# Kernel optimization log

Measured on AMD Instinct MI355X. Metric: run time of the kernel, lower is better.

## Reference

```python
import jax, jax.numpy as jnp
import numpy as np

N = 50000      # nodes
E = 800000     # edges (before self loops)
F_IN = 128     # input feature dim
H = 4          # attention heads
C = 64         # per-head channels (hidden_dim = out_channels = 64)
HC = H * C     # 256, concat output width of each GATv2Conv
G = 32         # number of graphs in the batch
NEG_SLOPE_ATT = 0.2   # GATv2 internal LeakyReLU
NEG_SLOPE_ACT = 0.01  # encoder nn.LeakyReLU() default


def _glorot(key, shape, fan_in):
    return jax.random.normal(key, shape, jnp.float32) * (1.0 / np.sqrt(fan_in))


def setup_inputs() -> dict:
    key = jax.random.key(0)
    ks = jax.random.split(key, 32)
    inp = {}
    inp["x"] = jax.random.normal(ks[0], (N, F_IN), jnp.float32)
    inp["edge_index"] = jax.random.randint(ks[1], (2, E), 0, N, jnp.int32)
    inp["batch"] = jnp.sort(jax.random.randint(ks[2], (N,), 0, G, jnp.int32))
    i = 3
    for li, fin in ((1, F_IN), (2, HC), (3, HC)):
        inp[f"Wl{li}"] = _glorot(ks[i], (HC, fin), fin); i += 1
        inp[f"bl{li}"] = jnp.zeros((HC,), jnp.float32)
        inp[f"Wr{li}"] = _glorot(ks[i], (HC, fin), fin); i += 1
        inp[f"br{li}"] = jnp.zeros((HC,), jnp.float32)
        inp[f"att{li}"] = _glorot(ks[i], (H, C), C); i += 1
        inp[f"bo{li}"] = jnp.zeros((HC,), jnp.float32)
    return inp


def _gatv2_layer(x, src, dst, Wl, bl, Wr, br, att, bo):
    n = x.shape[0]
    xl = (x @ Wl.T + bl).reshape(n, H, C)  # source transform
    xr = (x @ Wr.T + br).reshape(n, H, C)  # target transform
    # per-edge attention logits: a^T LeakyReLU(xl[j] + xr[i])
    e = jax.nn.leaky_relu(xl[src] + xr[dst], negative_slope=NEG_SLOPE_ATT)  # [E', H, C]
    score = jnp.einsum('ehc,hc->eh', e, att)                                # [E', H]
    # segment softmax over incoming edges of each destination node
    m = jax.ops.segment_max(score, dst, num_segments=n)
    p = jnp.exp(score - m[dst])
    s = jax.ops.segment_sum(p, dst, num_segments=n)
    alpha = p / s[dst]
    out = jax.ops.segment_sum(alpha[:, :, None] * xl[src], dst, num_segments=n)
    return out.reshape(n, HC) + bo


def reference(x, edge_index, batch,
              Wl1, bl1, Wr1, br1, att1, bo1,
              Wl2, bl2, Wr2, br2, att2, bo2,
              Wl3, bl3, Wr3, br3, att3, bo3):
    loop = jnp.arange(N, dtype=edge_index.dtype)
    src = jnp.concatenate([edge_index[0], loop])  # add self loops (PyG default)
    dst = jnp.concatenate([edge_index[1], loop])
    h = _gatv2_layer(x, src, dst, Wl1, bl1, Wr1, br1, att1, bo1)
    h = jax.nn.leaky_relu(h, negative_slope=NEG_SLOPE_ACT)
    h = _gatv2_layer(h, src, dst, Wl2, bl2, Wr2, br2, att2, bo2)
    h = jax.nn.leaky_relu(h, negative_slope=NEG_SLOPE_ACT)
    h = _gatv2_layer(h, src, dst, Wl3, bl3, Wr3, br3, att3, bo3)
    # global mean pool over graphs
    sums = jax.ops.segment_sum(h, batch, num_segments=G)
    cnt = jax.ops.segment_sum(jnp.ones((N,), h.dtype), batch, num_segments=G)
    return sums / jnp.maximum(cnt, 1.0)[:, None]
```

## Files before the change

kernel.cpp:

```cpp
#include <hip/hip_runtime.h>

#define HEADS 4
#define CH 64
#define HC 256
#define NGRAPH 32
#define NEG_ATT 0.2f
#define NEG_ACT 0.01f

typedef __attribute__((ext_vector_type(8))) short bf16x8;
typedef __attribute__((ext_vector_type(4))) float f32x4;

typedef __attribute__((address_space(3))) unsigned int lds_u32;
typedef const __attribute__((address_space(1))) unsigned int glob_u32;

__device__ __forceinline__ void gl_lds16(const void* g, void* l) {
  __builtin_amdgcn_global_load_lds((glob_u32*)(uintptr_t)g,
                                   (lds_u32*)(unsigned int)(uintptr_t)l, 16, 0, 0);
}

__device__ __forceinline__ void split2(float a, float b, unsigned& hi, unsigned& lo) {
  unsigned ua = __float_as_uint(a), ub = __float_as_uint(b);
  float la = a - __uint_as_float(ua & 0xFFFF0000u);
  float lb = b - __uint_as_float(ub & 0xFFFF0000u);
  hi = __builtin_amdgcn_perm(ub, ua, 0x07060302u);
  lo = __builtin_amdgcn_perm(__float_as_uint(lb), __float_as_uint(la), 0x07060302u);
}

__device__ __forceinline__ unsigned rtn_bf16(float f) {
  unsigned u = __float_as_uint(f);
  return (u + 0x7FFFu + ((u >> 16) & 1u)) >> 16;
}

__global__ __launch_bounds__(256) void convert_x(
    const float* __restrict__ X, unsigned short* __restrict__ xhi,
    unsigned short* __restrict__ xlo, int total4) {
  int g = blockIdx.x * 256 + threadIdx.x;
  if (g >= total4) return;
  float4 v = *(const float4*)&X[(size_t)g * 4];
  uint2 h2, l2;
  split2(v.x, v.y, h2.x, l2.x);
  split2(v.z, v.w, h2.y, l2.y);
  *(uint2*)&xhi[(size_t)g * 4] = h2;
  *(uint2*)&xlo[(size_t)g * 4] = l2;
}

__global__ __launch_bounds__(256) void convert_w_frag(
    const float* __restrict__ Wl, const float* __restrict__ Wr,
    unsigned short* __restrict__ wfhi, unsigned short* __restrict__ wflo, int K) {
  int g = blockIdx.x * 256 + threadIdx.x;
  int lane = g & 63;
  int ct = (g >> 6) & 31;
  int kb = g >> 11;
  int col = ct * 16 + (lane & 15);
  int k = kb * 32 + (lane >> 4) * 8;
  const float* src = (col < HC) ? &Wl[(size_t)col * K + k] : &Wr[(size_t)(col - HC) * K + k];
  float4 v0 = *(const float4*)src;
  float4 v1 = *(const float4*)(src + 4);
  uint4 hq, lq;
  split2(v0.x, v0.y, hq.x, lq.x);
  split2(v0.z, v0.w, hq.y, lq.y);
  split2(v1.x, v1.y, hq.z, lq.z);
  split2(v1.z, v1.w, hq.w, lq.w);
  *(uint4*)&wfhi[(size_t)g * 8] = hq;
  *(uint4*)&wflo[(size_t)g * 8] = lq;
}

__global__ __launch_bounds__(256) void gemm_fused(
    const unsigned short* __restrict__ xhi, const unsigned short* __restrict__ xlo,
    const unsigned short* __restrict__ wfhi, const unsigned short* __restrict__ wflo,
    const float* __restrict__ bl, const float* __restrict__ br,
    unsigned short* __restrict__ Y1, float* __restrict__ Y2, int N, int K) {
  __shared__ unsigned short Ah[2][128][32];
  __shared__ unsigned short Al[2][128][32];

  const int tid = threadIdx.x;
  const int wave = tid >> 6;
  const int lane = tid & 63;
  const int quad = lane >> 4;
  const int l16 = lane & 15;
  const int wr = (wave >> 1) * 64;
  const int wc = (wave & 1) * 64;
  const int col0 = blockIdx.x * 128;
  const int row0 = blockIdx.y * 128;
  const int ctg0 = blockIdx.x * 8 + (wave & 1) * 4;
  const int nkb = K >> 5;

  const int c0 = tid, c1 = tid + 256;
  const int r0g = row0 + (c0 >> 2), r1g = row0 + (c1 >> 2);
  const int ko0 = (c0 & 3) * 8, ko1 = (c1 & 3) * 8;
  const int gr0 = (r0g < N) ? r0g : N - 1;
  const int gr1 = (r1g < N) ? r1g : N - 1;

  f32x4 acc[4][4];
#pragma unroll
  for (int i = 0; i < 4; i++)
#pragma unroll
    for (int j = 0; j < 4; j++) acc[i][j] = (f32x4){0.f, 0.f, 0.f, 0.f};

  {
    size_t ga0 = (size_t)gr0 * K + ko0;
    size_t ga1 = (size_t)gr1 * K + ko1;
    gl_lds16(&xhi[ga0], &Ah[0][c0 >> 2][ko0]);
    gl_lds16(&xlo[ga0], &Al[0][c0 >> 2][ko0]);
    gl_lds16(&xhi[ga1], &Ah[0][c1 >> 2][ko1]);
    gl_lds16(&xlo[ga1], &Al[0][c1 >> 2][ko1]);
  }

  int p = 0;
  for (int kb = 0; kb < nkb; kb++) {
    bf16x8 bhi[4], blo[4];
#pragma unroll
    for (int j = 0; j < 4; j++) {
      size_t ci = ((size_t)kb * 32 + ctg0 + j) * 64 + lane;
      bhi[j] = *(const bf16x8*)&wfhi[ci * 8];
      blo[j] = *(const bf16x8*)&wflo[ci * 8];
    }
    __syncthreads();
    if (kb + 1 < nkb) {
      int k0 = (kb + 1) * 32;
      size_t ga0 = (size_t)gr0 * K + k0 + ko0;
      size_t ga1 = (size_t)gr1 * K + k0 + ko1;
      int q = p ^ 1;
      gl_lds16(&xhi[ga0], &Ah[q][c0 >> 2][ko0]);
      gl_lds16(&xlo[ga0], &Al[q][c0 >> 2][ko0]);
      gl_lds16(&xhi[ga1], &Ah[q][c1 >> 2][ko1]);
      gl_lds16(&xlo[ga1], &Al[q][c1 >> 2][ko1]);
    }
    bf16x8 ahi[4], alo[4];
#pragma unroll
    for (int i = 0; i < 4; i++) {
      ahi[i] = *(const bf16x8*)&Ah[p][wr + i * 16 + l16][quad * 8];
      alo[i] = *(const bf16x8*)&Al[p][wr + i * 16 + l16][quad * 8];
    }
#pragma unroll
    for (int i = 0; i < 4; i++)
#pragma unroll
      for (int j = 0; j < 4; j++) {
        acc[i][j] = __builtin_amdgcn_mfma_f32_16x16x32_bf16(ahi[i], bhi[j], acc[i][j], 0, 0, 0);
        acc[i][j] = __builtin_amdgcn_mfma_f32_16x16x32_bf16(ahi[i], blo[j], acc[i][j], 0, 0, 0);
        acc[i][j] = __builtin_amdgcn_mfma_f32_16x16x32_bf16(alo[i], bhi[j], acc[i][j], 0, 0, 0);
      }
    p ^= 1;
  }

#pragma unroll
  for (int j = 0; j < 4; j++) {
    int colg = col0 + wc + j * 16 + l16;
    if (colg < HC) {
      float bv = bl[colg];
#pragma unroll
      for (int i = 0; i < 4; i++)
#pragma unroll
        for (int r = 0; r < 4; r++) {
          int row = row0 + wr + i * 16 + quad * 4 + r;
          if (row < N)
            Y1[(size_t)row * HC + colg] = (unsigned short)rtn_bf16(acc[i][j][r] + bv);
        }
    } else {
      int cc = colg - HC;
      float bv = br[cc];
#pragma unroll
      for (int i = 0; i < 4; i++)
#pragma unroll
        for (int r = 0; r < 4; r++) {
          int row = row0 + wr + i * 16 + quad * 4 + r;
          if (row < N) Y2[(size_t)row * HC + cc] = acc[i][j][r] + bv;
        }
    }
  }
}

__global__ __launch_bounds__(256) void hist_dst(
    const int* __restrict__ edst, int* __restrict__ counts, int E) {
  int e = blockIdx.x * 256 + threadIdx.x;
  if (e < E) atomicAdd(&counts[edst[e]], 1);
}

__global__ __launch_bounds__(256) void scan_blocks(
    const int* __restrict__ counts, int* __restrict__ row_start,
    int* __restrict__ bsum, int N) {
  __shared__ int tmp[256];
  int t = threadIdx.x;
  int base = blockIdx.x * 1024 + t * 4;
  int v0 = (base     < N) ? counts[base]     + 1 : 0;
  int v1 = (base + 1 < N) ? counts[base + 1] + 1 : 0;
  int v2 = (base + 2 < N) ? counts[base + 2] + 1 : 0;
  int v3 = (base + 3 < N) ? counts[base + 3] + 1 : 0;
  int c1 = v0 + v1, c2 = c1 + v2, tot = c2 + v3;
  tmp[t] = tot;
  __syncthreads();
  for (int off = 1; off < 256; off <<= 1) {
    int add = (t >= off) ? tmp[t - off] : 0;
    __syncthreads();
    tmp[t] += add;
    __syncthreads();
  }
  int excl = tmp[t] - tot;
  if (base     < N) row_start[base + 1] = excl + v0;
  if (base + 1 < N) row_start[base + 2] = excl + c1;
  if (base + 2 < N) row_start[base + 3] = excl + c2;
  if (base + 3 < N) row_start[base + 4] = excl + tot;
  if (t == 255) bsum[blockIdx.x] = tmp[255];
  if (blockIdx.x == 0 && t == 0) row_start[0] = 0;
}

__global__ void scan_tops(int* __restrict__ bsum, int nb) {
  int lane = threadIdx.x;
  int v = (lane < nb) ? bsum[lane] : 0;
  for (int off = 1; off < 64; off <<= 1) {
    int u = __shfl_up(v, off);
    if (lane >= off) v += u;
  }
  if (lane < nb) bsum[lane] = v;
}

__global__ __launch_bounds__(256) void scan_add(
    int* __restrict__ row_start, const int* __restrict__ bsum, int N) {
  int off = bsum[blockIdx.x];
  int i = (blockIdx.x + 1) * 1024 + threadIdx.x * 4;
#pragma unroll
  for (int k = 0; k < 4; k++)
    if (i + k < N) row_start[i + k + 1] += off;
}

__global__ __launch_bounds__(256) void csr_init(
    const int* __restrict__ row_start, int* __restrict__ fill_pos,
    int* __restrict__ csr_src, int N) {
  int i = blockIdx.x * 256 + threadIdx.x;
  if (i < N) {
    int p = row_start[i];
    csr_src[p] = i;
    fill_pos[i] = p + 1;
  }
}

__global__ __launch_bounds__(256) void csr_scatter(
    const int* __restrict__ esrc, const int* __restrict__ edst,
    int* __restrict__ fill_pos, int* __restrict__ csr_src, int E) {
  int e = blockIdx.x * 256 + threadIdx.x;
  if (e < E) {
    int p = atomicAdd(&fill_pos[edst[e]], 1);
    csr_src[p] = esrc[e];
  }
}

__device__ __forceinline__ float4 unpack_bf16x4(uint2 q) {
  float4 r;
  r.x = __uint_as_float(q.x << 16);
  r.y = __uint_as_float(q.x & 0xFFFF0000u);
  r.z = __uint_as_float(q.y << 16);
  r.w = __uint_as_float(q.y & 0xFFFF0000u);
  return r;
}

__device__ __forceinline__ float edge_dot(const float4 lv, const float4 rv, const float4 a) {
  float t, d = 0.f;
  t = lv.x + rv.x; t = t > 0.f ? t : NEG_ATT * t; d = fmaf(t, a.x, d);
  t = lv.y + rv.y; t = t > 0.f ? t : NEG_ATT * t; d = fmaf(t, a.y, d);
  t = lv.z + rv.z; t = t > 0.f ? t : NEG_ATT * t; d = fmaf(t, a.z, d);
  t = lv.w + rv.w; t = t > 0.f ? t : NEG_ATT * t; d = fmaf(t, a.w, d);
  d += __shfl_xor(d, 1);
  d += __shfl_xor(d, 2);
  d += __shfl_xor(d, 4);
  d += __shfl_xor(d, 8);
  return d;
}

__global__ __launch_bounds__(256) void gat_fused(
    const unsigned short* __restrict__ xl, const float* __restrict__ xr,
    const int* __restrict__ row_start, const int* __restrict__ csr_src,
    const float* __restrict__ att, const float* __restrict__ bo,
    float* __restrict__ outf, unsigned short* __restrict__ ohi,
    unsigned short* __restrict__ olo, int N, int split_out) {
  int dst = (blockIdx.x * 256 + threadIdx.x) >> 6;
  int lane = threadIdx.x & 63;
  if (dst >= N) return;
  int h = lane >> 4;
  int off = h * CH + (lane & 15) * 4;
  const float4 a = *(const float4*)&att[off];
  const float4 rv = *(const float4*)&xr[(size_t)dst * HC + off];
  float4 o = {0.f, 0.f, 0.f, 0.f};
  float m = -__builtin_inff();
  float s = 0.f;
  int p = row_start[dst];
  int end = row_start[dst + 1];
  for (; p + 4 <= end; p += 4) {
    int s0 = csr_src[p + 0], s1 = csr_src[p + 1];
    int s2 = csr_src[p + 2], s3 = csr_src[p + 3];
    const float4 lv0 = unpack_bf16x4(*(const uint2*)&xl[(size_t)s0 * HC + off]);
    const float4 lv1 = unpack_bf16x4(*(const uint2*)&xl[(size_t)s1 * HC + off]);
    const float4 lv2 = unpack_bf16x4(*(const uint2*)&xl[(size_t)s2 * HC + off]);
    const float4 lv3 = unpack_bf16x4(*(const uint2*)&xl[(size_t)s3 * HC + off]);
    float d0 = edge_dot(lv0, rv, a);
    float d1 = edge_dot(lv1, rv, a);
    float d2 = edge_dot(lv2, rv, a);
    float d3 = edge_dot(lv3, rv, a);
    float newm = fmaxf(fmaxf(fmaxf(d0, d1), fmaxf(d2, d3)), m);
    float sc = __expf(m - newm);
    float e0 = __expf(d0 - newm), e1 = __expf(d1 - newm);
    float e2 = __expf(d2 - newm), e3 = __expf(d3 - newm);
    s = fmaf(s, sc, (e0 + e1) + (e2 + e3));
    o.x = fmaf(o.x, sc, fmaf(e0, lv0.x, fmaf(e1, lv1.x, fmaf(e2, lv2.x, e3 * lv3.x))));
    o.y = fmaf(o.y, sc, fmaf(e0, lv0.y, fmaf(e1, lv1.y, fmaf(e2, lv2.y, e3 * lv3.y))));
    o.z = fmaf(o.z, sc, fmaf(e0, lv0.z, fmaf(e1, lv1.z, fmaf(e2, lv2.z, e3 * lv3.z))));
    o.w = fmaf(o.w, sc, fmaf(e0, lv0.w, fmaf(e1, lv1.w, fmaf(e2, lv2.w, e3 * lv3.w))));
    m = newm;
  }
  for (; p < end; p++) {
    int src = csr_src[p];
    const float4 lv = unpack_bf16x4(*(const uint2*)&xl[(size_t)src * HC + off]);
    float d = edge_dot(lv, rv, a);
    float newm = fmaxf(m, d);
    float sc = __expf(m - newm);
    float pe = __expf(d - newm);
    s = fmaf(s, sc, pe);
    o.x = fmaf(o.x, sc, pe * lv.x);
    o.y = fmaf(o.y, sc, pe * lv.y);
    o.z = fmaf(o.z, sc, pe * lv.z);
    o.w = fmaf(o.w, sc, pe * lv.w);
    m = newm;
  }
  float inv = 1.f / s;
  const float4 b4 = *(const float4*)&bo[off];
  float4 res;
  res.x = fmaf(o.x, inv, b4.x);
  res.y = fmaf(o.y, inv, b4.y);
  res.z = fmaf(o.z, inv, b4.z);
  res.w = fmaf(o.w, inv, b4.w);
  if (split_out) {
    res.x = res.x > 0.f ? res.x : NEG_ACT * res.x;
    res.y = res.y > 0.f ? res.y : NEG_ACT * res.y;
    res.z = res.z > 0.f ? res.z : NEG_ACT * res.z;
    res.w = res.w > 0.f ? res.w : NEG_ACT * res.w;
    uint2 h2, l2;
    split2(res.x, res.y, h2.x, l2.x);
    split2(res.z, res.w, h2.y, l2.y);
    *(uint2*)&ohi[(size_t)dst * HC + off] = h2;
    *(uint2*)&olo[(size_t)dst * HC + off] = l2;
  } else {
    *(float4*)&outf[(size_t)dst * HC + off] = res;
  }
}

__global__ __launch_bounds__(256) void pool_partial(
    const float* __restrict__ h, const int* __restrict__ batch,
    float* __restrict__ out, int* __restrict__ cnt, int N) {
  __shared__ float part[NGRAPH][HC];
  __shared__ int bsh[256];
  __shared__ int cpart[NGRAPH];
  int j = threadIdx.x;
#pragma unroll
  for (int g = 0; g < NGRAPH; g++) part[g][j] = 0.f;
  if (j < NGRAPH) cpart[j] = 0;
  int n0 = blockIdx.x * 256;
  int nend = min(n0 + 256, N);
  int nj = n0 + j;
  bsh[j] = (nj < N) ? batch[nj] : 0;
  __syncthreads();
  if (nj < nend) atomicAdd(&cpart[bsh[j]], 1);
  for (int n = n0; n < nend; n++) {
    int g = bsh[n - n0];
    part[g][j] += h[(size_t)n * HC + j];
  }
  __syncthreads();
#pragma unroll
  for (int g = 0; g < NGRAPH; g++) {
    float v = part[g][j];
    if (v != 0.f) atomicAdd(&out[g * HC + j], v);
  }
  if (j < NGRAPH && cpart[j] > 0) atomicAdd(&cnt[j], cpart[j]);
}

__global__ __launch_bounds__(256) void pool_final(
    float* __restrict__ out, const int* __restrict__ cnt) {
  int g = blockIdx.x;
  int j = threadIdx.x;
  float c = (float)max(cnt[g], 1);
  out[g * HC + j] /= c;
}

extern "C" void kernel_launch(void* const* d_in, const int* in_sizes, int n_in,
                              void* d_out, int out_size, void* d_ws, size_t ws_size,
                              hipStream_t stream) {
  const float* x = (const float*)d_in[0];
  const int* ei = (const int*)d_in[1];
  const int* batch = (const int*)d_in[2];
  const int N = in_sizes[2];
  const int E = in_sizes[1] / 2;
  const int Etot = E + N;

  const float* Wl[3] = {(const float*)d_in[3], (const float*)d_in[9], (const float*)d_in[15]};
  const float* bl[3] = {(const float*)d_in[4], (const float*)d_in[10], (const float*)d_in[16]};
  const float* Wr[3] = {(const float*)d_in[5], (const float*)d_in[11], (const float*)d_in[17]};
  const float* br[3] = {(const float*)d_in[6], (const float*)d_in[12], (const float*)d_in[18]};
  const float* att[3] = {(const float*)d_in[7], (const float*)d_in[13], (const float*)d_in[19]};
  const float* bo[3] = {(const float*)d_in[8], (const float*)d_in[14], (const float*)d_in[20]};

  float* B0 = (float*)d_ws;
  float* B1 = B0 + (size_t)N * HC;
  float* B2 = B1 + (size_t)N * HC;
  unsigned short* w1hi = (unsigned short*)(B2 + (size_t)N * HC);
  unsigned short* w1lo = w1hi + 512 * 128;
  unsigned short* w2hi = w1lo + 512 * 128;
  unsigned short* w2lo = w2hi + 512 * 256;
  unsigned short* w3hi = w2lo + 512 * 256;
  unsigned short* w3lo = w3hi + 512 * 256;
  int* counts = (int*)(w3lo + 512 * 256);
  int* row_start = counts + N;
  int* bsum = row_start + N + 1;
  int* fill_pos = bsum + 64;
  int* csr_src = fill_pos + N;
  int* cnt = csr_src + Etot;

  unsigned short* xlB = (unsigned short*)B1;
  unsigned short* xhiL1 = (unsigned short*)B0;
  unsigned short* xloL1 = xhiL1 + (size_t)N * 128;
  unsigned short* xhiL = (unsigned short*)B0;
  unsigned short* xloL = xhiL + (size_t)N * HC;

  const int* esrc = ei;
  const int* edst = ei + E;

  convert_x<<<(N * 128 / 4 + 255) / 256, 256, 0, stream>>>(x, xhiL1, xloL1, N * 128 / 4);
  convert_w_frag<<<128 * 64 / 256, 256, 0, stream>>>(Wl[0], Wr[0], w1hi, w1lo, 128);
  convert_w_frag<<<256 * 64 / 256, 256, 0, stream>>>(Wl[1], Wr[1], w2hi, w2lo, 256);
  convert_w_frag<<<256 * 64 / 256, 256, 0, stream>>>(Wl[2], Wr[2], w3hi, w3lo, 256);

  const int nscan = (N + 1023) / 1024;
  (void)hipMemsetAsync(counts, 0, (size_t)N * sizeof(int), stream);
  hist_dst<<<(E + 255) / 256, 256, 0, stream>>>(edst, counts, E);
  scan_blocks<<<nscan, 256, 0, stream>>>(counts, row_start, bsum, N);
  scan_tops<<<1, 64, 0, stream>>>(bsum, nscan);
  scan_add<<<nscan - 1, 256, 0, stream>>>(row_start, bsum, N);
  csr_init<<<(N + 255) / 256, 256, 0, stream>>>(row_start, fill_pos, csr_src, N);
  csr_scatter<<<(E + 255) / 256, 256, 0, stream>>>(esrc, edst, fill_pos, csr_src, E);

  const dim3 ggrid(4, (N + 127) / 128);
  const int fblocks = (N * 64 + 255) / 256;

  gemm_fused<<<ggrid, 256, 0, stream>>>(xhiL1, xloL1, w1hi, w1lo, bl[0], br[0], xlB, B2, N, 128);
  gat_fused<<<fblocks, 256, 0, stream>>>(xlB, B2, row_start, csr_src, att[0], bo[0],
                                         nullptr, xhiL, xloL, N, 1);
  gemm_fused<<<ggrid, 256, 0, stream>>>(xhiL, xloL, w2hi, w2lo, bl[1], br[1], xlB, B2, N, 256);
  gat_fused<<<fblocks, 256, 0, stream>>>(xlB, B2, row_start, csr_src, att[1], bo[1],
                                         nullptr, xhiL, xloL, N, 1);
  gemm_fused<<<ggrid, 256, 0, stream>>>(xhiL, xloL, w3hi, w3lo, bl[2], br[2], xlB, B2, N, 256);
  gat_fused<<<fblocks, 256, 0, stream>>>(xlB, B2, row_start, csr_src, att[2], bo[2],
                                         B0, nullptr, nullptr, N, 0);

  (void)hipMemsetAsync(d_out, 0, NGRAPH * HC * sizeof(float), stream);
  (void)hipMemsetAsync(cnt, 0, NGRAPH * sizeof(int), stream);
  pool_partial<<<(N + 255) / 256, 256, 0, stream>>>(B0, batch, (float*)d_out, cnt, N);
  pool_final<<<NGRAPH, 256, 0, stream>>>((float*)d_out, cnt);
}
```

Baseline: 696.2 us.

## Prefetch GEMM weight fragments, template K, pre-scale CSR offsets, pack GAT math

The GEMM now takes K as a template parameter and fully unrolls the k-loop. Weight fragments for the next k-block are double-buffered in registers and loaded during the current block's MFMAs, to hide global load latency. The CSR source list stores byte offsets (src<<9) so the GAT gather skips the index multiply. The per-edge math is rewritten with float2 vectors and fmax-based LeakyReLU so the compiler can emit packed FP32 instructions. This raises register pressure in the GEMM, and the shifted offsets overflow int if N exceeds about 4M.

```diff
diff --git a/kernel.cpp b/kernel.cpp
--- a/kernel.cpp
+++ b/kernel.cpp
@@ -9,6 +9,7 @@
 
 typedef __attribute__((ext_vector_type(8))) short bf16x8;
 typedef __attribute__((ext_vector_type(4))) float f32x4;
+typedef __attribute__((ext_vector_type(2))) float f32x2;
 
 typedef __attribute__((address_space(3))) unsigned int lds_u32;
 typedef const __attribute__((address_space(1))) unsigned int glob_u32;
@@ -65,11 +66,13 @@
   *(uint4*)&wflo[(size_t)g * 8] = lq;
 }
 
+template <int K>
 __global__ __launch_bounds__(256) void gemm_fused(
     const unsigned short* __restrict__ xhi, const unsigned short* __restrict__ xlo,
     const unsigned short* __restrict__ wfhi, const unsigned short* __restrict__ wflo,
     const float* __restrict__ bl, const float* __restrict__ br,
-    unsigned short* __restrict__ Y1, float* __restrict__ Y2, int N, int K) {
+    unsigned short* __restrict__ Y1, float* __restrict__ Y2, int N) {
+  constexpr int nkb = K >> 5;
   __shared__ unsigned short Ah[2][128][32];
   __shared__ unsigned short Al[2][128][32];
 
@@ -83,7 +86,6 @@
   const int col0 = blockIdx.x * 128;
   const int row0 = blockIdx.y * 128;
   const int ctg0 = blockIdx.x * 8 + (wave & 1) * 4;
-  const int nkb = K >> 5;
 
   const int c0 = tid, c1 = tid + 256;
   const int r0g = row0 + (c0 >> 2), r1g = row0 + (c1 >> 2);
@@ -97,6 +99,13 @@
 #pragma unroll
     for (int j = 0; j < 4; j++) acc[i][j] = (f32x4){0.f, 0.f, 0.f, 0.f};
 
+  bf16x8 bhi[2][4], blo[2][4];
+#pragma unroll
+  for (int j = 0; j < 4; j++) {
+    size_t ci = (size_t)(ctg0 + j) * 64 + lane;
+    bhi[0][j] = *(const bf16x8*)&wfhi[ci * 8];
+    blo[0][j] = *(const bf16x8*)&wflo[ci * 8];
+  }
   {
     size_t ga0 = (size_t)gr0 * K + ko0;
     size_t ga1 = (size_t)gr1 * K + ko1;
@@ -106,41 +115,41 @@
     gl_lds16(&xlo[ga1], &Al[0][c1 >> 2][ko1]);
   }
 
-  int p = 0;
+#pragma unroll
   for (int kb = 0; kb < nkb; kb++) {
-    bf16x8 bhi[4], blo[4];
-#pragma unroll
-    for (int j = 0; j < 4; j++) {
-      size_t ci = ((size_t)kb * 32 + ctg0 + j) * 64 + lane;
-      bhi[j] = *(const bf16x8*)&wfhi[ci * 8];
-      blo[j] = *(const bf16x8*)&wflo[ci * 8];
-    }
+    const int cur = kb & 1, nxt = cur ^ 1;
     __syncthreads();
     if (kb + 1 < nkb) {
       int k0 = (kb + 1) * 32;
       size_t ga0 = (size_t)gr0 * K + k0 + ko0;
       size_t ga1 = (size_t)gr1 * K + k0 + ko1;
-      int q = p ^ 1;
-      gl_lds16(&xhi[ga0], &Ah[q][c0 >> 2][ko0]);
-      gl_lds16(&xlo[ga0], &Al[q][c0 >> 2][ko0]);
-      gl_lds16(&xhi[ga1], &Ah[q][c1 >> 2][ko1]);
-      gl_lds16(&xlo[ga1], &Al[q][c1 >> 2][ko1]);
+      gl_lds16(&xhi[ga0], &Ah[nxt][c0 >> 2][ko0]);
+      gl_lds16(&xlo[ga0], &Al[nxt][c0 >> 2][ko0]);
+      gl_lds16(&xhi[ga1], &Ah[nxt][c1 >> 2][ko1]);
+      gl_lds16(&xlo[ga1], &Al[nxt][c1 >> 2][ko1]);
     }
     bf16x8 ahi[4], alo[4];
 #pragma unroll
     for (int i = 0; i < 4; i++) {
-      ahi[i] = *(const bf16x8*)&Ah[p][wr + i * 16 + l16][quad * 8];
-      alo[i] = *(const bf16x8*)&Al[p][wr + i * 16 + l16][quad * 8];
+      ahi[i] = *(const bf16x8*)&Ah[cur][wr + i * 16 + l16][quad * 8];
+      alo[i] = *(const bf16x8*)&Al[cur][wr + i * 16 + l16][quad * 8];
     }
+    if (kb + 1 < nkb) {
+#pragma unroll
+      for (int j = 0; j < 4; j++) {
+        size_t ci = ((size_t)(kb + 1) * 32 + ctg0 + j) * 64 + lane;
+        bhi[nxt][j] = *(const bf16x8*)&wfhi[ci * 8];
+        blo[nxt][j] = *(const bf16x8*)&wflo[ci * 8];
+      }
+    }
 #pragma unroll
     for (int i = 0; i < 4; i++)
 #pragma unroll
       for (int j = 0; j < 4; j++) {
-        acc[i][j] = __builtin_amdgcn_mfma_f32_16x16x32_bf16(ahi[i], bhi[j], acc[i][j], 0, 0, 0);
-        acc[i][j] = __builtin_amdgcn_mfma_f32_16x16x32_bf16(ahi[i], blo[j], acc[i][j], 0, 0, 0);
-        acc[i][j] = __builtin_amdgcn_mfma_f32_16x16x32_bf16(alo[i], bhi[j], acc[i][j], 0, 0, 0);
+        acc[i][j] = __builtin_amdgcn_mfma_f32_16x16x32_bf16(ahi[i], bhi[cur][j], acc[i][j], 0, 0, 0);
+        acc[i][j] = __builtin_amdgcn_mfma_f32_16x16x32_bf16(ahi[i], blo[cur][j], acc[i][j], 0, 0, 0);
+        acc[i][j] = __builtin_amdgcn_mfma_f32_16x16x32_bf16(alo[i], bhi[cur][j], acc[i][j], 0, 0, 0);
       }
-    p ^= 1;
   }
 
 #pragma unroll
@@ -229,7 +238,7 @@
   int i = blockIdx.x * 256 + threadIdx.x;
   if (i < N) {
     int p = row_start[i];
-    csr_src[p] = i;
+    csr_src[p] = i << 9;
     fill_pos[i] = p + 1;
   }
 }
@@ -240,25 +249,25 @@
   int e = blockIdx.x * 256 + threadIdx.x;
   if (e < E) {
     int p = atomicAdd(&fill_pos[edst[e]], 1);
-    csr_src[p] = esrc[e];
-  }
-}
-
-__device__ __forceinline__ float4 unpack_bf16x4(uint2 q) {
-  float4 r;
-  r.x = __uint_as_float(q.x << 16);
-  r.y = __uint_as_float(q.x & 0xFFFF0000u);
-  r.z = __uint_as_float(q.y << 16);
-  r.w = __uint_as_float(q.y & 0xFFFF0000u);
-  return r;
-}
-
-__device__ __forceinline__ float edge_dot(const float4 lv, const float4 rv, const float4 a) {
-  float t, d = 0.f;
-  t = lv.x + rv.x; t = t > 0.f ? t : NEG_ATT * t; d = fmaf(t, a.x, d);
-  t = lv.y + rv.y; t = t > 0.f ? t : NEG_ATT * t; d = fmaf(t, a.y, d);
-  t = lv.z + rv.z; t = t > 0.f ? t : NEG_ATT * t; d = fmaf(t, a.z, d);
-  t = lv.w + rv.w; t = t > 0.f ? t : NEG_ATT * t; d = fmaf(t, a.w, d);
+    csr_src[p] = esrc[e] << 9;
+  }
+}
+
+__device__ __forceinline__ void unpk(uint2 q, f32x2& v01, f32x2& v23) {
+  v01.x = __uint_as_float(q.x << 16);
+  v01.y = __uint_as_float(q.x & 0xFFFF0000u);
+  v23.x = __uint_as_float(q.y << 16);
+  v23.y = __uint_as_float(q.y & 0xFFFF0000u);
+}
+
+__device__ __forceinline__ float edot(f32x2 l01, f32x2 l23, f32x2 r01, f32x2 r23,
+                                      f32x2 a01, f32x2 a23) {
+  f32x2 t01 = l01 + r01, t23 = l23 + r23;
+  f32x2 u01 = t01 * NEG_ATT, u23 = t23 * NEG_ATT;
+  t01.x = fmaxf(t01.x, u01.x); t01.y = fmaxf(t01.y, u01.y);
+  t23.x = fmaxf(t23.x, u23.x); t23.y = fmaxf(t23.y, u23.y);
+  f32x2 dv = t01 * a01 + t23 * a23;
+  float d = dv.x + dv.y;
   d += __shfl_xor(d, 1);
   d += __shfl_xor(d, 2);
   d += __shfl_xor(d, 4);
@@ -268,7 +277,7 @@
 
 __global__ __launch_bounds__(256) void gat_fused(
     const unsigned short* __restrict__ xl, const float* __restrict__ xr,
-    const int* __restrict__ row_start, const int* __restrict__ csr_src,
+    const int* __restrict__ row_start, const int* __restrict__ csr_soff,
     const float* __restrict__ att, const float* __restrict__ bo,
     float* __restrict__ outf, unsigned short* __restrict__ ohi,
     unsigned short* __restrict__ olo, int N, int split_out) {
@@ -277,68 +286,79 @@
   if (dst >= N) return;
   int h = lane >> 4;
   int off = h * CH + (lane & 15) * 4;
-  const float4 a = *(const float4*)&att[off];
-  const float4 rv = *(const float4*)&xr[(size_t)dst * HC + off];
-  float4 o = {0.f, 0.f, 0.f, 0.f};
+  const int loff = off * 2;
+  const char* xlc = (const char*)xl;
+  f32x2 a01 = *(const f32x2*)&att[off];
+  f32x2 a23 = *(const f32x2*)&att[off + 2];
+  f32x2 r01 = *(const f32x2*)&xr[(size_t)dst * HC + off];
+  f32x2 r23 = *(const f32x2*)&xr[(size_t)dst * HC + off + 2];
+  f32x2 o01 = {0.f, 0.f}, o23 = {0.f, 0.f};
   float m = -__builtin_inff();
   float s = 0.f;
   int p = row_start[dst];
   int end = row_start[dst + 1];
   for (; p + 4 <= end; p += 4) {
-    int s0 = csr_src[p + 0], s1 = csr_src[p + 1];
-    int s2 = csr_src[p + 2], s3 = csr_src[p + 3];
-    const float4 lv0 = unpack_bf16x4(*(const uint2*)&xl[(size_t)s0 * HC + off]);
-    const float4 lv1 = unpack_bf16x4(*(const uint2*)&xl[(size_t)s1 * HC + off]);
-    const float4 lv2 = unpack_bf16x4(*(const uint2*)&xl[(size_t)s2 * HC + off]);
-    const float4 lv3 = unpack_bf16x4(*(const uint2*)&xl[(size_t)s3 * HC + off]);
-    float d0 = edge_dot(lv0, rv, a);
-    float d1 = edge_dot(lv1, rv, a);
-    float d2 = edge_dot(lv2, rv, a);
-    float d3 = edge_dot(lv3, rv, a);
+    int b0 = csr_soff[p + 0] + loff, b1 = csr_soff[p + 1] + loff;
+    int b2 = csr_soff[p + 2] + loff, b3 = csr_soff[p + 3] + loff;
+    uint2 q0 = *(const uint2*)(xlc + b0);
+    uint2 q1 = *(const uint2*)(xlc + b1);
+    uint2 q2 = *(const uint2*)(xlc + b2);
+    uint2 q3 = *(const uint2*)(xlc + b3);
+    f32x2 l0a, l0b, l1a, l1b, l2a, l2b, l3a, l3b;
+    unpk(q0, l0a, l0b);
+    unpk(q1, l1a, l1b);
+    unpk(q2, l2a, l2b);
+    unpk(q3, l3a, l3b);
+    float d0 = edot(l0a, l0b, r01, r23, a01, a23);
+    float d1 = edot(l1a, l1b, r01, r23, a01, a23);
+    float d2 = edot(l2a, l2b, r01, r23, a01, a23);
+    float d3 = edot(l3a, l3b, r01, r23, a01, a23);
     float newm = fmaxf(fmaxf(fmaxf(d0, d1), fmaxf(d2, d3)), m);
     float sc = __expf(m - newm);
     float e0 = __expf(d0 - newm), e1 = __expf(d1 - newm);
     float e2 = __expf(d2 - newm), e3 = __expf(d3 - newm);
     s = fmaf(s, sc, (e0 + e1) + (e2 + e3));
-    o.x = fmaf(o.x, sc, fmaf(e0, lv0.x, fmaf(e1, lv1.x, fmaf(e2, lv2.x, e3 * lv3.x))));
-    o.y = fmaf(o.y, sc, fmaf(e0, lv0.y, fmaf(e1, lv1.y, fmaf(e2, lv2.y, e3 * lv3.y))));
-    o.z = fmaf(o.z, sc, fmaf(e0, lv0.z, fmaf(e1, lv1.z, fmaf(e2, lv2.z, e3 * lv3.z))));
-    o.w = fmaf(o.w, sc, fmaf(e0, lv0.w, fmaf(e1, lv1.w, fmaf(e2, lv2.w, e3 * lv3.w))));
+    f32x2 acc01 = l0a * e0 + l1a * e1;
+    acc01 = l2a * e2 + acc01;
+    acc01 = l3a * e3 + acc01;
+    o01 = o01 * sc + acc01;
+    f32x2 acc23 = l0b * e0 + l1b * e1;
+    acc23 = l2b * e2 + acc23;
+    acc23 = l3b * e3 + acc23;
+    o23 = o23 * sc + acc23;
     m = newm;
   }
   for (; p < end; p++) {
-    int src = csr_src[p];
-    const float4 lv = unpack_bf16x4(*(const uint2*)&xl[(size_t)src * HC + off]);
-    float d = edge_dot(lv, rv, a);
+    int b0 = csr_soff[p] + loff;
+    uint2 q0 = *(const uint2*)(xlc + b0);
+    f32x2 la, lb;
+    unpk(q0, la, lb);
+    float d = edot(la, lb, r01, r23, a01, a23);
     float newm = fmaxf(m, d);
     float sc = __expf(m - newm);
     float pe = __expf(d - newm);
     s = fmaf(s, sc, pe);
-    o.x = fmaf(o.x, sc, pe * lv.x);
-    o.y = fmaf(o.y, sc, pe * lv.y);
-    o.z = fmaf(o.z, sc, pe * lv.z);
-    o.w = fmaf(o.w, sc, pe * lv.w);
+    o01 = o01 * sc + la * pe;
+    o23 = o23 * sc + lb * pe;
     m = newm;
   }
   float inv = 1.f / s;
-  const float4 b4 = *(const float4*)&bo[off];
-  float4 res;
-  res.x = fmaf(o.x, inv, b4.x);
-  res.y = fmaf(o.y, inv, b4.y);
-  res.z = fmaf(o.z, inv, b4.z);
-  res.w = fmaf(o.w, inv, b4.w);
+  f32x2 b01 = *(const f32x2*)&bo[off];
+  f32x2 b23 = *(const f32x2*)&bo[off + 2];
+  f32x2 res01 = o01 * inv + b01;
+  f32x2 res23 = o23 * inv + b23;
   if (split_out) {
-    res.x = res.x > 0.f ? res.x : NEG_ACT * res.x;
-    res.y = res.y > 0.f ? res.y : NEG_ACT * res.y;
-    res.z = res.z > 0.f ? res.z : NEG_ACT * res.z;
-    res.w = res.w > 0.f ? res.w : NEG_ACT * res.w;
+    f32x2 v01 = res01 * NEG_ACT, v23 = res23 * NEG_ACT;
+    res01.x = fmaxf(res01.x, v01.x); res01.y = fmaxf(res01.y, v01.y);
+    res23.x = fmaxf(res23.x, v23.x); res23.y = fmaxf(res23.y, v23.y);
     uint2 h2, l2;
-    split2(res.x, res.y, h2.x, l2.x);
-    split2(res.z, res.w, h2.y, l2.y);
+    split2(res01.x, res01.y, h2.x, l2.x);
+    split2(res23.x, res23.y, h2.y, l2.y);
     *(uint2*)&ohi[(size_t)dst * HC + off] = h2;
     *(uint2*)&olo[(size_t)dst * HC + off] = l2;
   } else {
-    *(float4*)&outf[(size_t)dst * HC + off] = res;
+    float4 r4 = {res01.x, res01.y, res23.x, res23.y};
+    *(float4*)&outf[(size_t)dst * HC + off] = r4;
   }
 }
 
@@ -438,13 +458,13 @@
   const dim3 ggrid(4, (N + 127) / 128);
   const int fblocks = (N * 64 + 255) / 256;
 
-  gemm_fused<<<ggrid, 256, 0, stream>>>(xhiL1, xloL1, w1hi, w1lo, bl[0], br[0], xlB, B2, N, 128);
+  gemm_fused<128><<<ggrid, 256, 0, stream>>>(xhiL1, xloL1, w1hi, w1lo, bl[0], br[0], xlB, B2, N);
   gat_fused<<<fblocks, 256, 0, stream>>>(xlB, B2, row_start, csr_src, att[0], bo[0],
                                          nullptr, xhiL, xloL, N, 1);
-  gemm_fused<<<ggrid, 256, 0, stream>>>(xhiL, xloL, w2hi, w2lo, bl[1], br[1], xlB, B2, N, 256);
+  gemm_fused<256><<<ggrid, 256, 0, stream>>>(xhiL, xloL, w2hi, w2lo, bl[1], br[1], xlB, B2, N);
   gat_fused<<<fblocks, 256, 0, stream>>>(xlB, B2, row_start, csr_src, att[1], bo[1],
                                          nullptr, xhiL, xloL, N, 1);
-  gemm_fused<<<ggrid, 256, 0, stream>>>(xhiL, xloL, w3hi, w3lo, bl[2], br[2], xlB, B2, N, 256);
+  gemm_fused<256><<<ggrid, 256, 0, stream>>>(xhiL, xloL, w3hi, w3lo, bl[2], br[2], xlB, B2, N);
   gat_fused<<<fblocks, 256, 0, stream>>>(xlB, B2, row_start, csr_src, att[2], bo[2],
                                          B0, nullptr, nullptr, N, 0);
 
```

After: 692.1 us. Within noise of the previous version (-0.6%).
